# Kernel tuning notes

Measured on AMD Instinct MI355X. Metric: run time of the kernel, lower is better.

Reference implementation:

```python
import jax, jax.numpy as jnp
import numpy as np

B, T, D, U = 32, 4096, 256, 256


def setup_inputs() -> dict:
    key = jax.random.key(0)
    ks = jax.random.split(key, 5)
    s = 1.0 / np.sqrt(D)
    return {
        "query": jax.random.normal(ks[0], (B, D), jnp.float32),
        "values": jax.random.normal(ks[1], (B, T, D), jnp.float32),
        "W1": jax.random.normal(ks[2], (D, U), jnp.float32) * s,
        "b1": jnp.zeros((U,), jnp.float32),
        "W2": jax.random.normal(ks[3], (D, U), jnp.float32) * s,
        "b2": jnp.zeros((U,), jnp.float32),
        "V": jax.random.normal(ks[4], (U, 1), jnp.float32) * (1.0 / np.sqrt(U)),
        "bV": jnp.zeros((1,), jnp.float32),
    }


def reference(query, values, W1, b1, W2, b2, V, bV):
    # score[b,t,u] = tanh(values @ W1 + b1 + (query @ W2 + b2)[:,None,:])
    proj_v = jnp.einsum("btd,du->btu", values, W1) + b1        # [B,T,U]
    proj_q = (query @ W2 + b2)[:, None, :]                      # [B,1,U]
    score = jnp.tanh(proj_v + proj_q) @ V + bV                  # [B,T,1]
    attn = jax.nn.softmax(score, axis=1)                        # softmax over T
    context = jnp.sum(attn * values, axis=1)                    # [B,D]
    return (context, attn)
```

## Files before the change

kernel.cpp:

```cpp
#include <hip/hip_runtime.h>
#include <hip/hip_bf16.h>

typedef __attribute__((ext_vector_type(4))) float f32x4;
typedef __attribute__((ext_vector_type(8))) short s16x8;
typedef __attribute__((ext_vector_type(4))) short s16x4;

static constexpr int Bn = 32;
static constexpr int Tn = 4096;
static constexpr int Dn = 256;
static constexpr int Un = 256;
static constexpr int CH = Tn / 64;

__device__ __forceinline__ ushort f2bf_hw(float f) {
    union { __hip_bfloat16 h; ushort u; } c;
    c.h = __float2bfloat16(f);
    return c.u;
}
__device__ __forceinline__ float bf2f(ushort u) {
    return __uint_as_float(((unsigned)u) << 16);
}
__device__ __forceinline__ float tanh5(float x) {
    float t = __expf(2.0f * x);
    return 1.0f - __fdividef(2.0f, 1.0f + t);
}

__global__ __launch_bounds__(256) void k_prep(const float* __restrict__ W1,
                                              ushort* __restrict__ W1T,
                                              const float* __restrict__ query,
                                              const float* __restrict__ W2,
                                              const float* __restrict__ b1,
                                              const float* __restrict__ b2,
                                              float* __restrict__ qb) {
    __shared__ float qs[Dn];
    if (blockIdx.x < 256) {
        const int u = blockIdx.x, d = threadIdx.x;
        W1T[u * Dn + d] = f2bf_hw(W1[d * Un + u]);
    } else {
        const int b = blockIdx.x - 256, u = threadIdx.x;
        qs[u] = query[b * Dn + u];
        __syncthreads();
        float acc = b1[u] + b2[u];
        #pragma unroll 8
        for (int d = 0; d < Dn; ++d) acc += qs[d] * W2[d * Un + u];
        qb[b * Un + u] = acc;
    }
}

__global__ __launch_bounds__(256, 4) void k_fused(const float* __restrict__ values,
                                                  const ushort* __restrict__ W1T,
                                                  const float* __restrict__ qb,
                                                  const float* __restrict__ Vw,
                                                  const float* __restrict__ bV,
                                                  float* __restrict__ scores,
                                                  float* __restrict__ pm,
                                                  float* __restrict__ ps,
                                                  float* __restrict__ pctx) {
    __shared__ __align__(16) ushort Al[64][264];
    __shared__ float sred[4][64];
    __shared__ f32x4 cred[4][64];
    const int tid = threadIdx.x;
    const int b = blockIdx.y, c = blockIdx.x;
    const int t0 = c * 64;
    const int wid = tid >> 6, lane = tid & 63;
    const int l15 = lane & 15, hi = lane >> 4;

    const float* vbase = values + ((size_t)b * Tn + t0) * Dn;
    #pragma unroll
    for (int i = 0; i < 8; ++i) {
        int flat = i * 2048 + tid * 8;
        int row = flat >> 8, col = flat & 255;
        const float4 f0 = *(const float4*)&vbase[row * Dn + col];
        const float4 f1 = *(const float4*)&vbase[row * Dn + col + 4];
        s16x8 p;
        p[0] = (short)f2bf_hw(f0.x); p[1] = (short)f2bf_hw(f0.y);
        p[2] = (short)f2bf_hw(f0.z); p[3] = (short)f2bf_hw(f0.w);
        p[4] = (short)f2bf_hw(f1.x); p[5] = (short)f2bf_hw(f1.y);
        p[6] = (short)f2bf_hw(f1.z); p[7] = (short)f2bf_hw(f1.w);
        *(s16x8*)&Al[row][col] = p;
    }

    const ushort* wbase = W1T + (size_t)(wid * 64 + l15) * Dn + hi * 8;

    f32x4 acc[4][4];
    #pragma unroll
    for (int tt = 0; tt < 4; ++tt)
        #pragma unroll
        for (int ut = 0; ut < 4; ++ut) acc[tt][ut] = (f32x4){0.f, 0.f, 0.f, 0.f};

    s16x8 bfn0[4], bfn1[4];
    #pragma unroll
    for (int ut = 0; ut < 4; ++ut)
        bfn0[ut] = *(const s16x8*)&wbase[(size_t)ut * 16 * Dn];
    #pragma unroll
    for (int ut = 0; ut < 4; ++ut)
        bfn1[ut] = *(const s16x8*)&wbase[(size_t)ut * 16 * Dn + 32];

    __syncthreads();

    #pragma unroll
    for (int kc = 0; kc < 8; ++kc) {
        s16x8 bf[4];
        #pragma unroll
        for (int ut = 0; ut < 4; ++ut) { bf[ut] = bfn0[ut]; bfn0[ut] = bfn1[ut]; }
        if (kc < 6) {
            #pragma unroll
            for (int ut = 0; ut < 4; ++ut)
                bfn1[ut] = *(const s16x8*)&wbase[(size_t)ut * 16 * Dn + (kc + 2) * 32];
        }
        const int k0 = kc * 32;
        s16x8 af[4];
        #pragma unroll
        for (int tt = 0; tt < 4; ++tt)
            af[tt] = *(const s16x8*)&Al[tt * 16 + l15][k0 + hi * 8];
        #pragma unroll
        for (int tt = 0; tt < 4; ++tt)
            #pragma unroll
            for (int ut = 0; ut < 4; ++ut)
                acc[tt][ut] = __builtin_amdgcn_mfma_f32_16x16x32_bf16(af[tt], bf[ut], acc[tt][ut], 0, 0, 0);
    }

    float Vreg[4], qreg[4];
    #pragma unroll
    for (int ut = 0; ut < 4; ++ut) {
        int u = wid * 64 + ut * 16 + l15;
        Vreg[ut] = Vw[u];
        qreg[ut] = qb[b * Un + u];
    }

    float psc[4][4];
    #pragma unroll
    for (int tt = 0; tt < 4; ++tt)
        #pragma unroll
        for (int i = 0; i < 4; ++i) psc[tt][i] = 0.f;
    #pragma unroll
    for (int tt = 0; tt < 4; ++tt)
        #pragma unroll
        for (int ut = 0; ut < 4; ++ut)
            #pragma unroll
            for (int i = 0; i < 4; ++i)
                psc[tt][i] += tanh5(acc[tt][ut][i] + qreg[ut]) * Vreg[ut];

    #pragma unroll
    for (int tt = 0; tt < 4; ++tt)
        #pragma unroll
        for (int i = 0; i < 4; ++i) {
            float v = psc[tt][i];
            v += __shfl_xor(v, 1, 64);
            v += __shfl_xor(v, 2, 64);
            v += __shfl_xor(v, 4, 64);
            v += __shfl_xor(v, 8, 64);
            if (l15 == 0) sred[wid][tt * 16 + hi * 4 + i] = v;
        }
    __syncthreads();

    float s = sred[0][lane] + sred[1][lane] + sred[2][lane] + sred[3][lane] + bV[0];
    if (wid == 0) scores[b * Tn + t0 + lane] = s;
    float m = s;
    #pragma unroll
    for (int off = 32; off > 0; off >>= 1) m = fmaxf(m, __shfl_xor(m, off, 64));
    const float p = __expf(s - m);
    float S = p;
    #pragma unroll
    for (int off = 32; off > 0; off >>= 1) S += __shfl_xor(S, off, 64);

    const int d4 = lane * 4;
    f32x4 loc = (f32x4){0.f, 0.f, 0.f, 0.f};
    #pragma unroll
    for (int k = 0; k < 16; ++k) {
        const int t = wid + 4 * k;
        const float pk = __shfl(p, t, 64);
        const s16x4 v = *(const s16x4*)&Al[t][d4];
        loc[0] += pk * bf2f((ushort)v[0]);
        loc[1] += pk * bf2f((ushort)v[1]);
        loc[2] += pk * bf2f((ushort)v[2]);
        loc[3] += pk * bf2f((ushort)v[3]);
    }
    cred[wid][lane] = loc;
    __syncthreads();
    if (wid == 0) {
        const f32x4 o = cred[0][lane] + cred[1][lane] + cred[2][lane] + cred[3][lane];
        *(f32x4*)&pctx[((size_t)(b * CH + c)) * Dn + d4] = o;
    }
    if (tid == 0) { pm[b * CH + c] = m; ps[b * CH + c] = S; }
}

__global__ __launch_bounds__(256) void k_reduce(const float* __restrict__ pm,
                                                const float* __restrict__ ps,
                                                const float* __restrict__ pctx,
                                                float* __restrict__ context,
                                                float* __restrict__ MS) {
    const int b = blockIdx.x, d = threadIdx.x;
    float M = -1e30f;
    #pragma unroll 8
    for (int c = 0; c < CH; ++c) M = fmaxf(M, pm[b * CH + c]);
    float S = 0.f, ctx = 0.f;
    #pragma unroll 4
    for (int c = 0; c < CH; ++c) {
        const float w = __expf(pm[b * CH + c] - M);
        S += w * ps[b * CH + c];
        ctx += w * pctx[((size_t)(b * CH + c)) * Dn + d];
    }
    context[b * Dn + d] = __fdividef(ctx, S);
    if (d == 0) { MS[b * 2] = M; MS[b * 2 + 1] = S; }
}

__global__ __launch_bounds__(256) void k_attn(float* __restrict__ attn,
                                              const float* __restrict__ MS) {
    const int b = blockIdx.y;
    const int base = b * Tn + blockIdx.x * 1024 + threadIdx.x * 4;
    const float M = MS[b * 2];
    const float invS = __fdividef(1.0f, MS[b * 2 + 1]);
    float4 s = *(const float4*)&attn[base];
    s.x = __expf(s.x - M) * invS;
    s.y = __expf(s.y - M) * invS;
    s.z = __expf(s.z - M) * invS;
    s.w = __expf(s.w - M) * invS;
    *(float4*)&attn[base] = s;
}

extern "C" void kernel_launch(void* const* d_in, const int* in_sizes, int n_in,
                              void* d_out, int out_size, void* d_ws, size_t ws_size,
                              hipStream_t stream) {
    const float* query  = (const float*)d_in[0];
    const float* values = (const float*)d_in[1];
    const float* W1     = (const float*)d_in[2];
    const float* b1     = (const float*)d_in[3];
    const float* W2     = (const float*)d_in[4];
    const float* b2     = (const float*)d_in[5];
    const float* Vw     = (const float*)d_in[6];
    const float* bV     = (const float*)d_in[7];

    float* context = (float*)d_out;
    float* attn    = (float*)d_out + Bn * Dn;

    float*  pctx = (float*)d_ws;
    float*  pm   = pctx + (size_t)Bn * CH * Dn;
    float*  ps   = pm + Bn * CH;
    float*  qb   = ps + Bn * CH;
    float*  MS   = qb + Bn * Un;
    ushort* W1T  = (ushort*)(MS + Bn * 2);

    k_prep<<<dim3(256 + Bn), dim3(256), 0, stream>>>(W1, W1T, query, W2, b1, b2, qb);
    k_fused<<<dim3(CH, Bn), dim3(256), 0, stream>>>(values, W1T, qb, Vw, bV,
                                                    attn, pm, ps, pctx);
    k_reduce<<<dim3(Bn), dim3(256), 0, stream>>>(pm, ps, pctx, context, MS);
    k_attn<<<dim3(Tn / 1024, Bn), dim3(256), 0, stream>>>(attn, MS);
}
```

Before: 78.82 us.

## Split fused attention block across eight waves with 2x4 MFMA wave grid

Doubles the fused kernel's block to 512 threads and arranges waves as a 2x4 grid over time rows and units, halving per-wave MFMA tiles and accumulators. The values load, context accumulation and reduction are redistributed over eight waves, with an extra barrier to fold the context partials. The W1 prefetch depth drops from two stages to one. The aim is more waves in flight to hide global load latency, at the cost of an extra sync and tighter register limits from the new launch bounds.

```diff
diff --git a/kernel.cpp b/kernel.cpp
--- a/kernel.cpp
+++ b/kernel.cpp
@@ -46,7 +46,7 @@
     }
 }
 
-__global__ __launch_bounds__(256, 4) void k_fused(const float* __restrict__ values,
+__global__ __launch_bounds__(512, 6) void k_fused(const float* __restrict__ values,
                                                   const ushort* __restrict__ W1T,
                                                   const float* __restrict__ qb,
                                                   const float* __restrict__ Vw,
@@ -63,11 +63,12 @@
     const int t0 = c * 64;
     const int wid = tid >> 6, lane = tid & 63;
     const int l15 = lane & 15, hi = lane >> 4;
+    const int wr = wid >> 2, wc = wid & 3;
 
     const float* vbase = values + ((size_t)b * Tn + t0) * Dn;
     #pragma unroll
-    for (int i = 0; i < 8; ++i) {
-        int flat = i * 2048 + tid * 8;
+    for (int i = 0; i < 4; ++i) {
+        int flat = i * 4096 + tid * 8;
         int row = flat >> 8, col = flat & 255;
         const float4 f0 = *(const float4*)&vbase[row * Dn + col];
         const float4 f1 = *(const float4*)&vbase[row * Dn + col + 4];
@@ -79,61 +80,59 @@
         *(s16x8*)&Al[row][col] = p;
     }
 
-    const ushort* wbase = W1T + (size_t)(wid * 64 + l15) * Dn + hi * 8;
-
-    f32x4 acc[4][4];
-    #pragma unroll
-    for (int tt = 0; tt < 4; ++tt)
+    const ushort* wbase = W1T + (size_t)(wc * 64 + l15) * Dn + hi * 8;
+
+    f32x4 acc[2][4];
+    #pragma unroll
+    for (int tt = 0; tt < 2; ++tt)
         #pragma unroll
         for (int ut = 0; ut < 4; ++ut) acc[tt][ut] = (f32x4){0.f, 0.f, 0.f, 0.f};
 
-    s16x8 bfn0[4], bfn1[4];
+    s16x8 bcur[4], bnxt[4];
     #pragma unroll
     for (int ut = 0; ut < 4; ++ut)
-        bfn0[ut] = *(const s16x8*)&wbase[(size_t)ut * 16 * Dn];
-    #pragma unroll
-    for (int ut = 0; ut < 4; ++ut)
-        bfn1[ut] = *(const s16x8*)&wbase[(size_t)ut * 16 * Dn + 32];
+        bcur[ut] = *(const s16x8*)&wbase[(size_t)ut * 16 * Dn];
 
     __syncthreads();
 
     #pragma unroll
     for (int kc = 0; kc < 8; ++kc) {
-        s16x8 bf[4];
-        #pragma unroll
-        for (int ut = 0; ut < 4; ++ut) { bf[ut] = bfn0[ut]; bfn0[ut] = bfn1[ut]; }
-        if (kc < 6) {
+        if (kc < 7) {
             #pragma unroll
             for (int ut = 0; ut < 4; ++ut)
-                bfn1[ut] = *(const s16x8*)&wbase[(size_t)ut * 16 * Dn + (kc + 2) * 32];
+                bnxt[ut] = *(const s16x8*)&wbase[(size_t)ut * 16 * Dn + (kc + 1) * 32];
         }
         const int k0 = kc * 32;
-        s16x8 af[4];
-        #pragma unroll
-        for (int tt = 0; tt < 4; ++tt)
-            af[tt] = *(const s16x8*)&Al[tt * 16 + l15][k0 + hi * 8];
-        #pragma unroll
-        for (int tt = 0; tt < 4; ++tt)
+        s16x8 af[2];
+        #pragma unroll
+        for (int tt = 0; tt < 2; ++tt)
+            af[tt] = *(const s16x8*)&Al[wr * 32 + tt * 16 + l15][k0 + hi * 8];
+        #pragma unroll
+        for (int tt = 0; tt < 2; ++tt)
             #pragma unroll
             for (int ut = 0; ut < 4; ++ut)
-                acc[tt][ut] = __builtin_amdgcn_mfma_f32_16x16x32_bf16(af[tt], bf[ut], acc[tt][ut], 0, 0, 0);
+                acc[tt][ut] = __builtin_amdgcn_mfma_f32_16x16x32_bf16(af[tt], bcur[ut], acc[tt][ut], 0, 0, 0);
+        if (kc < 7) {
+            #pragma unroll
+            for (int ut = 0; ut < 4; ++ut) bcur[ut] = bnxt[ut];
+        }
     }
 
     float Vreg[4], qreg[4];
     #pragma unroll
     for (int ut = 0; ut < 4; ++ut) {
-        int u = wid * 64 + ut * 16 + l15;
+        int u = wc * 64 + ut * 16 + l15;
         Vreg[ut] = Vw[u];
         qreg[ut] = qb[b * Un + u];
     }
 
-    float psc[4][4];
-    #pragma unroll
-    for (int tt = 0; tt < 4; ++tt)
+    float psc[2][4];
+    #pragma unroll
+    for (int tt = 0; tt < 2; ++tt)
         #pragma unroll
         for (int i = 0; i < 4; ++i) psc[tt][i] = 0.f;
     #pragma unroll
-    for (int tt = 0; tt < 4; ++tt)
+    for (int tt = 0; tt < 2; ++tt)
         #pragma unroll
         for (int ut = 0; ut < 4; ++ut)
             #pragma unroll
@@ -141,7 +140,7 @@
                 psc[tt][i] += tanh5(acc[tt][ut][i] + qreg[ut]) * Vreg[ut];
 
     #pragma unroll
-    for (int tt = 0; tt < 4; ++tt)
+    for (int tt = 0; tt < 2; ++tt)
         #pragma unroll
         for (int i = 0; i < 4; ++i) {
             float v = psc[tt][i];
@@ -149,7 +148,7 @@
             v += __shfl_xor(v, 2, 64);
             v += __shfl_xor(v, 4, 64);
             v += __shfl_xor(v, 8, 64);
-            if (l15 == 0) sred[wid][tt * 16 + hi * 4 + i] = v;
+            if (l15 == 0) sred[wc][wr * 32 + tt * 16 + hi * 4 + i] = v;
         }
     __syncthreads();
 
@@ -166,8 +165,8 @@
     const int d4 = lane * 4;
     f32x4 loc = (f32x4){0.f, 0.f, 0.f, 0.f};
     #pragma unroll
-    for (int k = 0; k < 16; ++k) {
-        const int t = wid + 4 * k;
+    for (int k = 0; k < 8; ++k) {
+        const int t = wid + 8 * k;
         const float pk = __shfl(p, t, 64);
         const s16x4 v = *(const s16x4*)&Al[t][d4];
         loc[0] += pk * bf2f((ushort)v[0]);
@@ -175,7 +174,12 @@
         loc[2] += pk * bf2f((ushort)v[2]);
         loc[3] += pk * bf2f((ushort)v[3]);
     }
-    cred[wid][lane] = loc;
+    if (wid < 4) cred[wid][lane] = loc;
+    __syncthreads();
+    if (wid >= 4) {
+        f32x4 t = cred[wid - 4][lane];
+        cred[wid - 4][lane] = t + loc;
+    }
     __syncthreads();
     if (wid == 0) {
         const f32x4 o = cred[0][lane] + cred[1][lane] + cred[2][lane] + cred[3][lane];
@@ -241,7 +245,7 @@
     ushort* W1T  = (ushort*)(MS + Bn * 2);
 
     k_prep<<<dim3(256 + Bn), dim3(256), 0, stream>>>(W1, W1T, query, W2, b1, b2, qb);
-    k_fused<<<dim3(CH, Bn), dim3(256), 0, stream>>>(values, W1T, qb, Vw, bV,
+    k_fused<<<dim3(CH, Bn), dim3(512), 0, stream>>>(values, W1T, qb, Vw, bV,
                                                     attn, pm, ps, pctx);
     k_reduce<<<dim3(Bn), dim3(256), 0, stream>>>(pm, ps, pctx, context, MS);
     k_attn<<<dim3(Tn / 1024, Bn), dim3(256), 0, stream>>>(attn, MS);
```

Result: slower. 96.48 us (+22.4%).

## Make each wave process its own 16-row tile independently without block barriers

Applied to the files above, without the earlier changes.

Restructures the fused kernel so each wave loads, converts and scores its own 16 timesteps against all 256 units. It then writes its own softmax partial (max, sum, context) with no __syncthreads anywhere in the block. This removes block-wide barriers and cross-wave LDS reductions so waves can overlap memory and compute freely. In exchange, every wave streams the whole bf16 W1T instead of a quarter of it, roughly quadrupling L2 traffic for weights. There are also four times as many partials for k_reduce to combine serially over only 32 blocks.

```diff
diff --git a/kernel.cpp b/kernel.cpp
--- a/kernel.cpp
+++ b/kernel.cpp
@@ -10,6 +10,7 @@
 static constexpr int Dn = 256;
 static constexpr int Un = 256;
 static constexpr int CH = Tn / 64;
+static constexpr int NP = CH * 4;
 
 __device__ __forceinline__ ushort f2bf_hw(float f) {
     union { __hip_bfloat16 h; ushort u; } c;
@@ -46,28 +47,27 @@
     }
 }
 
-__global__ __launch_bounds__(256, 4) void k_fused(const float* __restrict__ values,
-                                                  const ushort* __restrict__ W1T,
-                                                  const float* __restrict__ qb,
-                                                  const float* __restrict__ Vw,
-                                                  const float* __restrict__ bV,
-                                                  float* __restrict__ scores,
-                                                  float* __restrict__ pm,
-                                                  float* __restrict__ ps,
-                                                  float* __restrict__ pctx) {
-    __shared__ __align__(16) ushort Al[64][264];
-    __shared__ float sred[4][64];
-    __shared__ f32x4 cred[4][64];
+__global__ __launch_bounds__(256, 4) void k_free(const float* __restrict__ values,
+                                                 const ushort* __restrict__ W1T,
+                                                 const float* __restrict__ qb,
+                                                 const float* __restrict__ Vw,
+                                                 const float* __restrict__ bV,
+                                                 float* __restrict__ scores,
+                                                 float* __restrict__ pm,
+                                                 float* __restrict__ ps,
+                                                 float* __restrict__ pctx) {
+    __shared__ __align__(16) ushort Al[4][16][264];
+    __shared__ float slp[4][16];
     const int tid = threadIdx.x;
     const int b = blockIdx.y, c = blockIdx.x;
-    const int t0 = c * 64;
     const int wid = tid >> 6, lane = tid & 63;
     const int l15 = lane & 15, hi = lane >> 4;
+    const int t0 = c * 64 + wid * 16;
 
     const float* vbase = values + ((size_t)b * Tn + t0) * Dn;
     #pragma unroll
-    for (int i = 0; i < 8; ++i) {
-        int flat = i * 2048 + tid * 8;
+    for (int j = 0; j < 8; ++j) {
+        int flat = j * 512 + lane * 8;
         int row = flat >> 8, col = flat & 255;
         const float4 f0 = *(const float4*)&vbase[row * Dn + col];
         const float4 f1 = *(const float4*)&vbase[row * Dn + col + 4];
@@ -76,112 +76,96 @@
         p[2] = (short)f2bf_hw(f0.z); p[3] = (short)f2bf_hw(f0.w);
         p[4] = (short)f2bf_hw(f1.x); p[5] = (short)f2bf_hw(f1.y);
         p[6] = (short)f2bf_hw(f1.z); p[7] = (short)f2bf_hw(f1.w);
-        *(s16x8*)&Al[row][col] = p;
-    }
-
-    const ushort* wbase = W1T + (size_t)(wid * 64 + l15) * Dn + hi * 8;
-
-    f32x4 acc[4][4];
-    #pragma unroll
-    for (int tt = 0; tt < 4; ++tt)
+        *(s16x8*)&Al[wid][row][col] = p;
+    }
+
+    f32x4 acc[16];
+    #pragma unroll
+    for (int ut = 0; ut < 16; ++ut) acc[ut] = (f32x4){0.f, 0.f, 0.f, 0.f};
+
+    const ushort* wb = W1T + (size_t)l15 * Dn + hi * 8;
+    s16x8 bq[4], bn[4];
+    #pragma unroll
+    for (int j = 0; j < 4; ++j)
+        bq[j] = *(const s16x8*)&wb[(size_t)j * 16 * Dn];
+
+    s16x8 afc = *(const s16x8*)&Al[wid][l15][hi * 8];
+    s16x8 afn;
+
+    #pragma unroll
+    for (int kc = 0; kc < 8; ++kc) {
+        if (kc < 7) afn = *(const s16x8*)&Al[wid][l15][(kc + 1) * 32 + hi * 8];
         #pragma unroll
-        for (int ut = 0; ut < 4; ++ut) acc[tt][ut] = (f32x4){0.f, 0.f, 0.f, 0.f};
-
-    s16x8 bfn0[4], bfn1[4];
-    #pragma unroll
-    for (int ut = 0; ut < 4; ++ut)
-        bfn0[ut] = *(const s16x8*)&wbase[(size_t)ut * 16 * Dn];
-    #pragma unroll
-    for (int ut = 0; ut < 4; ++ut)
-        bfn1[ut] = *(const s16x8*)&wbase[(size_t)ut * 16 * Dn + 32];
-
-    __syncthreads();
-
-    #pragma unroll
-    for (int kc = 0; kc < 8; ++kc) {
-        s16x8 bf[4];
+        for (int q = 0; q < 4; ++q) {
+            const int nk = (q == 3) ? kc + 1 : kc;
+            const int nq = (q + 1) & 3;
+            if (!(kc == 7 && q == 3)) {
+                #pragma unroll
+                for (int j = 0; j < 4; ++j)
+                    bn[j] = *(const s16x8*)&wb[(size_t)(nq * 4 + j) * 16 * Dn + nk * 32];
+            }
+            #pragma unroll
+            for (int j = 0; j < 4; ++j)
+                acc[q * 4 + j] = __builtin_amdgcn_mfma_f32_16x16x32_bf16(afc, bq[j], acc[q * 4 + j], 0, 0, 0);
+            #pragma unroll
+            for (int j = 0; j < 4; ++j) bq[j] = bn[j];
+        }
+        afc = afn;
+    }
+
+    float psc[4] = {0.f, 0.f, 0.f, 0.f};
+    #pragma unroll
+    for (int ut = 0; ut < 16; ++ut) {
+        const int u = ut * 16 + l15;
+        const float Vv = Vw[u];
+        const float qv = qb[b * Un + u];
         #pragma unroll
-        for (int ut = 0; ut < 4; ++ut) { bf[ut] = bfn0[ut]; bfn0[ut] = bfn1[ut]; }
-        if (kc < 6) {
-            #pragma unroll
-            for (int ut = 0; ut < 4; ++ut)
-                bfn1[ut] = *(const s16x8*)&wbase[(size_t)ut * 16 * Dn + (kc + 2) * 32];
-        }
-        const int k0 = kc * 32;
-        s16x8 af[4];
+        for (int i = 0; i < 4; ++i)
+            psc[i] += tanh5(acc[ut][i] + qv) * Vv;
+    }
+    #pragma unroll
+    for (int i = 0; i < 4; ++i) {
+        float v = psc[i];
+        v += __shfl_xor(v, 1, 64);
+        v += __shfl_xor(v, 2, 64);
+        v += __shfl_xor(v, 4, 64);
+        v += __shfl_xor(v, 8, 64);
+        psc[i] = v;
+    }
+    const float bv = bV[0];
+    if (l15 == 0) {
         #pragma unroll
-        for (int tt = 0; tt < 4; ++tt)
-            af[tt] = *(const s16x8*)&Al[tt * 16 + l15][k0 + hi * 8];
-        #pragma unroll
-        for (int tt = 0; tt < 4; ++tt)
-            #pragma unroll
-            for (int ut = 0; ut < 4; ++ut)
-                acc[tt][ut] = __builtin_amdgcn_mfma_f32_16x16x32_bf16(af[tt], bf[ut], acc[tt][ut], 0, 0, 0);
-    }
-
-    float Vreg[4], qreg[4];
-    #pragma unroll
-    for (int ut = 0; ut < 4; ++ut) {
-        int u = wid * 64 + ut * 16 + l15;
-        Vreg[ut] = Vw[u];
-        qreg[ut] = qb[b * Un + u];
-    }
-
-    float psc[4][4];
-    #pragma unroll
-    for (int tt = 0; tt < 4; ++tt)
-        #pragma unroll
-        for (int i = 0; i < 4; ++i) psc[tt][i] = 0.f;
-    #pragma unroll
-    for (int tt = 0; tt < 4; ++tt)
-        #pragma unroll
-        for (int ut = 0; ut < 4; ++ut)
-            #pragma unroll
-            for (int i = 0; i < 4; ++i)
-                psc[tt][i] += tanh5(acc[tt][ut][i] + qreg[ut]) * Vreg[ut];
-
-    #pragma unroll
-    for (int tt = 0; tt < 4; ++tt)
-        #pragma unroll
-        for (int i = 0; i < 4; ++i) {
-            float v = psc[tt][i];
-            v += __shfl_xor(v, 1, 64);
-            v += __shfl_xor(v, 2, 64);
-            v += __shfl_xor(v, 4, 64);
-            v += __shfl_xor(v, 8, 64);
-            if (l15 == 0) sred[wid][tt * 16 + hi * 4 + i] = v;
-        }
-    __syncthreads();
-
-    float s = sred[0][lane] + sred[1][lane] + sred[2][lane] + sred[3][lane] + bV[0];
-    if (wid == 0) scores[b * Tn + t0 + lane] = s;
-    float m = s;
-    #pragma unroll
-    for (int off = 32; off > 0; off >>= 1) m = fmaxf(m, __shfl_xor(m, off, 64));
-    const float p = __expf(s - m);
+        for (int i = 0; i < 4; ++i) slp[wid][hi * 4 + i] = psc[i] + bv;
+    }
+    float sr = slp[wid][l15];
+    if (hi == 0) scores[b * Tn + t0 + l15] = sr;
+    float m = sr;
+    m = fmaxf(m, __shfl_xor(m, 1, 64));
+    m = fmaxf(m, __shfl_xor(m, 2, 64));
+    m = fmaxf(m, __shfl_xor(m, 4, 64));
+    m = fmaxf(m, __shfl_xor(m, 8, 64));
+    const float p = __expf(sr - m);
     float S = p;
-    #pragma unroll
-    for (int off = 32; off > 0; off >>= 1) S += __shfl_xor(S, off, 64);
+    S += __shfl_xor(S, 1, 64);
+    S += __shfl_xor(S, 2, 64);
+    S += __shfl_xor(S, 4, 64);
+    S += __shfl_xor(S, 8, 64);
+    if (hi == 0) slp[wid][l15] = p;
 
     const int d4 = lane * 4;
     f32x4 loc = (f32x4){0.f, 0.f, 0.f, 0.f};
     #pragma unroll
-    for (int k = 0; k < 16; ++k) {
-        const int t = wid + 4 * k;
-        const float pk = __shfl(p, t, 64);
-        const s16x4 v = *(const s16x4*)&Al[t][d4];
+    for (int t = 0; t < 16; ++t) {
+        const float pk = slp[wid][t];
+        const s16x4 v = *(const s16x4*)&Al[wid][t][d4];
         loc[0] += pk * bf2f((ushort)v[0]);
         loc[1] += pk * bf2f((ushort)v[1]);
         loc[2] += pk * bf2f((ushort)v[2]);
         loc[3] += pk * bf2f((ushort)v[3]);
     }
-    cred[wid][lane] = loc;
-    __syncthreads();
-    if (wid == 0) {
-        const f32x4 o = cred[0][lane] + cred[1][lane] + cred[2][lane] + cred[3][lane];
-        *(f32x4*)&pctx[((size_t)(b * CH + c)) * Dn + d4] = o;
-    }
-    if (tid == 0) { pm[b * CH + c] = m; ps[b * CH + c] = S; }
+    const int pp = (b * CH + c) * 4 + wid;
+    *(f32x4*)&pctx[(size_t)pp * Dn + d4] = loc;
+    if (lane == 0) { pm[pp] = m; ps[pp] = S; }
 }
 
 __global__ __launch_bounds__(256) void k_reduce(const float* __restrict__ pm,
@@ -192,13 +176,13 @@
     const int b = blockIdx.x, d = threadIdx.x;
     float M = -1e30f;
     #pragma unroll 8
-    for (int c = 0; c < CH; ++c) M = fmaxf(M, pm[b * CH + c]);
+    for (int c = 0; c < NP; ++c) M = fmaxf(M, pm[b * NP + c]);
     float S = 0.f, ctx = 0.f;
     #pragma unroll 4
-    for (int c = 0; c < CH; ++c) {
-        const float w = __expf(pm[b * CH + c] - M);
-        S += w * ps[b * CH + c];
-        ctx += w * pctx[((size_t)(b * CH + c)) * Dn + d];
+    for (int c = 0; c < NP; ++c) {
+        const float w = __expf(pm[b * NP + c] - M);
+        S += w * ps[b * NP + c];
+        ctx += w * pctx[((size_t)(b * NP + c)) * Dn + d];
     }
     context[b * Dn + d] = __fdividef(ctx, S);
     if (d == 0) { MS[b * 2] = M; MS[b * 2 + 1] = S; }
@@ -234,15 +218,15 @@
     float* attn    = (float*)d_out + Bn * Dn;
 
     float*  pctx = (float*)d_ws;
-    float*  pm   = pctx + (size_t)Bn * CH * Dn;
-    float*  ps   = pm + Bn * CH;
-    float*  qb   = ps + Bn * CH;
+    float*  pm   = pctx + (size_t)Bn * NP * Dn;
+    float*  ps   = pm + Bn * NP;
+    float*  qb   = ps + Bn * NP;
     float*  MS   = qb + Bn * Un;
     ushort* W1T  = (ushort*)(MS + Bn * 2);
 
     k_prep<<<dim3(256 + Bn), dim3(256), 0, stream>>>(W1, W1T, query, W2, b1, b2, qb);
-    k_fused<<<dim3(CH, Bn), dim3(256), 0, stream>>>(values, W1T, qb, Vw, bV,
-                                                    attn, pm, ps, pctx);
+    k_free<<<dim3(CH, Bn), dim3(256), 0, stream>>>(values, W1T, qb, Vw, bV,
+                                                   attn, pm, ps, pctx);
     k_reduce<<<dim3(Bn), dim3(256), 0, stream>>>(pm, ps, pctx, context, MS);
     k_attn<<<dim3(Tn / 1024, Bn), dim3(256), 0, stream>>>(attn, MS);
 }
```

Measured after the change: 184.3 us. 134% more time.

## Pre-swizzle W1 into MFMA fragment order and swap operand roles

Applied to the files above, without the earlier changes.

Replaces the W1 transpose with a prep kernel that writes bf16 W1 directly in per-lane MFMA fragment order, so each wave reads its B fragments as fully contiguous 16-byte-per-lane loads. The MFMA operands are swapped so U runs along rows, which lets the tanh·V epilogue use float4 loads of V and qb and reduce across only two shuffle steps instead of four. The prep is split into two kernels, adding one launch, and the register prefetch depth drops from two stages to one.

```diff
diff --git a/kernel.cpp b/kernel.cpp
--- a/kernel.cpp
+++ b/kernel.cpp
@@ -24,30 +24,37 @@
     return 1.0f - __fdividef(2.0f, 1.0f + t);
 }
 
-__global__ __launch_bounds__(256) void k_prep(const float* __restrict__ W1,
-                                              ushort* __restrict__ W1T,
-                                              const float* __restrict__ query,
-                                              const float* __restrict__ W2,
-                                              const float* __restrict__ b1,
-                                              const float* __restrict__ b2,
-                                              float* __restrict__ qb) {
+__global__ __launch_bounds__(256) void k_w1f(const float* __restrict__ W1,
+                                             ushort* __restrict__ W1F) {
+    const int g = blockIdx.x * 256 + threadIdx.x;
+    const int f = g >> 6, lane = g & 63;
+    const int kc = f & 7, ut = (f >> 3) & 3, wc = f >> 5;
+    const int u = wc * 64 + ut * 16 + (lane & 15);
+    const int d0 = kc * 32 + (lane >> 4) * 8;
+    s16x8 p;
+    #pragma unroll
+    for (int j = 0; j < 8; ++j)
+        p[j] = (short)f2bf_hw(W1[(size_t)(d0 + j) * Un + u]);
+    *(s16x8*)&W1F[(size_t)g * 8] = p;
+}
+
+__global__ __launch_bounds__(256) void k_qproj(const float* __restrict__ query,
+                                               const float* __restrict__ W2,
+                                               const float* __restrict__ b1,
+                                               const float* __restrict__ b2,
+                                               float* __restrict__ qb) {
     __shared__ float qs[Dn];
-    if (blockIdx.x < 256) {
-        const int u = blockIdx.x, d = threadIdx.x;
-        W1T[u * Dn + d] = f2bf_hw(W1[d * Un + u]);
-    } else {
-        const int b = blockIdx.x - 256, u = threadIdx.x;
-        qs[u] = query[b * Dn + u];
-        __syncthreads();
-        float acc = b1[u] + b2[u];
-        #pragma unroll 8
-        for (int d = 0; d < Dn; ++d) acc += qs[d] * W2[d * Un + u];
-        qb[b * Un + u] = acc;
-    }
+    const int b = blockIdx.x, u = threadIdx.x;
+    qs[u] = query[b * Dn + u];
+    __syncthreads();
+    float acc = b1[u] + b2[u];
+    #pragma unroll 8
+    for (int d = 0; d < Dn; ++d) acc += qs[d] * W2[d * Un + u];
+    qb[b * Un + u] = acc;
 }
 
 __global__ __launch_bounds__(256, 4) void k_fused(const float* __restrict__ values,
-                                                  const ushort* __restrict__ W1T,
+                                                  const ushort* __restrict__ W1F,
                                                   const float* __restrict__ qb,
                                                   const float* __restrict__ Vw,
                                                   const float* __restrict__ bV,
@@ -79,33 +86,27 @@
         *(s16x8*)&Al[row][col] = p;
     }
 
-    const ushort* wbase = W1T + (size_t)(wid * 64 + l15) * Dn + hi * 8;
+    const ushort* wf = W1F + (size_t)wid * 32 * 512 + lane * 8;
 
     f32x4 acc[4][4];
     #pragma unroll
-    for (int tt = 0; tt < 4; ++tt)
-        #pragma unroll
-        for (int ut = 0; ut < 4; ++ut) acc[tt][ut] = (f32x4){0.f, 0.f, 0.f, 0.f};
-
-    s16x8 bfn0[4], bfn1[4];
-    #pragma unroll
     for (int ut = 0; ut < 4; ++ut)
-        bfn0[ut] = *(const s16x8*)&wbase[(size_t)ut * 16 * Dn];
+        #pragma unroll
+        for (int tt = 0; tt < 4; ++tt) acc[ut][tt] = (f32x4){0.f, 0.f, 0.f, 0.f};
+
+    s16x8 wcur[4], wnxt[4];
     #pragma unroll
     for (int ut = 0; ut < 4; ++ut)
-        bfn1[ut] = *(const s16x8*)&wbase[(size_t)ut * 16 * Dn + 32];
+        wcur[ut] = *(const s16x8*)&wf[(size_t)(ut * 8) * 512];
 
     __syncthreads();
 
     #pragma unroll
     for (int kc = 0; kc < 8; ++kc) {
-        s16x8 bf[4];
-        #pragma unroll
-        for (int ut = 0; ut < 4; ++ut) { bf[ut] = bfn0[ut]; bfn0[ut] = bfn1[ut]; }
-        if (kc < 6) {
+        if (kc < 7) {
             #pragma unroll
             for (int ut = 0; ut < 4; ++ut)
-                bfn1[ut] = *(const s16x8*)&wbase[(size_t)ut * 16 * Dn + (kc + 2) * 32];
+                wnxt[ut] = *(const s16x8*)&wf[(size_t)(ut * 8 + kc + 1) * 512];
         }
         const int k0 = kc * 32;
         s16x8 af[4];
@@ -113,44 +114,38 @@
         for (int tt = 0; tt < 4; ++tt)
             af[tt] = *(const s16x8*)&Al[tt * 16 + l15][k0 + hi * 8];
         #pragma unroll
-        for (int tt = 0; tt < 4; ++tt)
-            #pragma unroll
-            for (int ut = 0; ut < 4; ++ut)
-                acc[tt][ut] = __builtin_amdgcn_mfma_f32_16x16x32_bf16(af[tt], bf[ut], acc[tt][ut], 0, 0, 0);
-    }
-
-    float Vreg[4], qreg[4];
-    #pragma unroll
-    for (int ut = 0; ut < 4; ++ut) {
-        int u = wid * 64 + ut * 16 + l15;
-        Vreg[ut] = Vw[u];
-        qreg[ut] = qb[b * Un + u];
-    }
-
-    float psc[4][4];
-    #pragma unroll
-    for (int tt = 0; tt < 4; ++tt)
-        #pragma unroll
-        for (int i = 0; i < 4; ++i) psc[tt][i] = 0.f;
-    #pragma unroll
-    for (int tt = 0; tt < 4; ++tt)
-        #pragma unroll
         for (int ut = 0; ut < 4; ++ut)
             #pragma unroll
-            for (int i = 0; i < 4; ++i)
-                psc[tt][i] += tanh5(acc[tt][ut][i] + qreg[ut]) * Vreg[ut];
-
-    #pragma unroll
-    for (int tt = 0; tt < 4; ++tt)
-        #pragma unroll
-        for (int i = 0; i < 4; ++i) {
-            float v = psc[tt][i];
-            v += __shfl_xor(v, 1, 64);
-            v += __shfl_xor(v, 2, 64);
-            v += __shfl_xor(v, 4, 64);
-            v += __shfl_xor(v, 8, 64);
-            if (l15 == 0) sred[wid][tt * 16 + hi * 4 + i] = v;
+            for (int tt = 0; tt < 4; ++tt)
+                acc[ut][tt] = __builtin_amdgcn_mfma_f32_16x16x32_bf16(wcur[ut], af[tt], acc[ut][tt], 0, 0, 0);
+        if (kc < 7) {
+            #pragma unroll
+            for (int ut = 0; ut < 4; ++ut) wcur[ut] = wnxt[ut];
         }
+    }
+
+    float4 Vq[4], qq[4];
+    #pragma unroll
+    for (int ut = 0; ut < 4; ++ut) {
+        const int u0 = wid * 64 + ut * 16 + hi * 4;
+        Vq[ut] = *(const float4*)&Vw[u0];
+        qq[ut] = *(const float4*)&qb[b * Un + u0];
+    }
+
+    #pragma unroll
+    for (int tt = 0; tt < 4; ++tt) {
+        float v = 0.f;
+        #pragma unroll
+        for (int ut = 0; ut < 4; ++ut) {
+            v += tanh5(acc[ut][tt][0] + qq[ut].x) * Vq[ut].x;
+            v += tanh5(acc[ut][tt][1] + qq[ut].y) * Vq[ut].y;
+            v += tanh5(acc[ut][tt][2] + qq[ut].z) * Vq[ut].z;
+            v += tanh5(acc[ut][tt][3] + qq[ut].w) * Vq[ut].w;
+        }
+        v += __shfl_xor(v, 16, 64);
+        v += __shfl_xor(v, 32, 64);
+        if (hi == 0) sred[wid][tt * 16 + l15] = v;
+    }
     __syncthreads();
 
     float s = sred[0][lane] + sred[1][lane] + sred[2][lane] + sred[3][lane] + bV[0];
@@ -238,10 +233,11 @@
     float*  ps   = pm + Bn * CH;
     float*  qb   = ps + Bn * CH;
     float*  MS   = qb + Bn * Un;
-    ushort* W1T  = (ushort*)(MS + Bn * 2);
-
-    k_prep<<<dim3(256 + Bn), dim3(256), 0, stream>>>(W1, W1T, query, W2, b1, b2, qb);
-    k_fused<<<dim3(CH, Bn), dim3(256), 0, stream>>>(values, W1T, qb, Vw, bV,
+    ushort* W1F  = (ushort*)(MS + Bn * 2);
+
+    k_w1f<<<dim3(32), dim3(256), 0, stream>>>(W1, W1F);
+    k_qproj<<<dim3(Bn), dim3(256), 0, stream>>>(query, W2, b1, b2, qb);
+    k_fused<<<dim3(CH, Bn), dim3(256), 0, stream>>>(values, W1F, qb, Vw, bV,
                                                     attn, pm, ps, pctx);
     k_reduce<<<dim3(Bn), dim3(256), 0, stream>>>(pm, ps, pctx, context, MS);
     k_attn<<<dim3(Tn / 1024, Bn), dim3(256), 0, stream>>>(attn, MS);
```

Measured after the change: 77.22 us. 2.0% less time.
